# Optimization experiments

Hardware: AMD Instinct MI355X
Metric: run time of the kernel (lower is better)

Reference implementation:

```python
import jax, jax.numpy as jnp
import numpy as np

B, C, H, W = 8, 64, 256, 256
M1, M2 = 16, 16


def setup_inputs() -> dict:
    key = jax.random.key(0)
    k1, k2, k3 = jax.random.split(key, 3)
    scale = 1.0 / (C * C)
    x = jax.random.normal(k1, (B, C, H, W), dtype=jnp.float32)
    # torch.rand(..., dtype=cfloat) -> uniform [0,1) real and imag parts
    w_real = scale * jax.random.uniform(k2, (C, C, M1, M2), dtype=jnp.float32)
    w_imag = scale * jax.random.uniform(k3, (C, C, M1, M2), dtype=jnp.float32)
    return {"x": x, "w_real": w_real, "w_imag": w_imag}


def reference(x, w_real, w_imag):
    m1, m2 = w_real.shape[2], w_real.shape[3]
    h, w = x.shape[-2], x.shape[-1]
    weights = w_real + 1j * w_imag  # (Cin, Cout, m1, m2) complex64
    # rfftn over axes (-1,-2): real->complex transform on the LAST listed axis (-2),
    # so x_ft has shape (B, C, H//2+1, W) — matching torch exactly.
    x_ft = jnp.fft.rfftn(x, axes=(-1, -2))
    out_low = jnp.einsum('bixy,ioxy->boxy', x_ft[..., :m1, :m2], weights)
    out_ft = jnp.zeros_like(x_ft).at[..., :m1, :m2].set(out_low)
    # irfftn with s=(H,W) over default axes (-2,-1): irfft on the last axis
    # truncates it to W//2+1 — same quirky-but-valid behavior as the torch code.
    return jnp.fft.irfftn(out_ft, s=(h, w))
```

## Files before the change

kernel.cpp:

```cpp
#include <hip/hip_runtime.h>
#include <math.h>

#define NIMG 512
#define HW   65536

__global__ __launch_bounds__(256)
void twinit(float* __restrict__ tw_g) {
    int idx = blockIdx.x * 256 + threadIdx.x;
    int n = idx >> 4, k = idx & 15;
    float s, c;
    sincospif(((k * n) & 255) * (1.0f / 128.0f), &s, &c);
    tw_g[idx * 2]     = c;
    tw_g[idx * 2 + 1] = s;
}

__global__ __launch_bounds__(256, 4)
void stageA(const float* __restrict__ x, const float* __restrict__ tw_g,
            float* __restrict__ xf_re, float* __restrict__ xf_im) {
    __shared__ __attribute__((aligned(16))) float tw[2048];
    __shared__ __attribute__((aligned(16))) float cbuf[8192];
    const int tid = threadIdx.x;
    const int img = blockIdx.x;

    ((float4*)tw)[tid]       = ((const float4*)tw_g)[tid];
    ((float4*)tw)[tid + 256] = ((const float4*)tw_g)[tid + 256];
    __syncthreads();

    const float* xp = x + (size_t)img * HW + tid;
    float cr[16], ci[16];
    #pragma unroll
    for (int u = 0; u < 16; ++u) { cr[u] = 0.0f; ci[u] = 0.0f; }

    const float4* tw4 = (const float4*)tw;
    #pragma unroll 2
    for (int hb = 0; hb < 64; ++hb) {
        float a = xp[hb * 256];
        float b = xp[(hb + 64) * 256];
        float c = xp[(hb + 128) * 256];
        float d = xp[(hb + 192) * 256];
        float p = a + c, m = a - c, q = b + d, r = b - d;
        float s0 = p + q, s2 = p - q;
        #pragma unroll
        for (int qq = 0; qq < 8; ++qq) {
            float4 e = tw4[hb * 8 + qq];
            float se = (qq & 1) ? s2 : s0;
            float si = (qq & 1) ? r : -r;
            cr[2*qq]     += se * e.x;
            ci[2*qq]     -= se * e.y;
            cr[2*qq + 1] += m  * e.z + si * e.w;
            ci[2*qq + 1] += si * e.z - m  * e.w;
        }
    }

    float2* cb = (float2*)cbuf;
    #pragma unroll
    for (int u = 0; u < 16; ++u)
        cb[u * 256 + tid] = make_float2(cr[u], ci[u]);
    __syncthreads();

    const int u = tid >> 4, v = tid & 15;
    const bool odd = (v & 1) != 0;
    const float t = (v & 2) ? -1.0f : 1.0f;
    const float2* twc = (const float2*)tw;
    float xr = 0.0f, xi = 0.0f;
    #pragma unroll 2
    for (int wb = 0; wb < 64; ++wb) {
        float2 Ca = cb[u * 256 + wb];
        float2 Cb = cb[u * 256 + wb + 64];
        float2 Cc = cb[u * 256 + wb + 128];
        float2 Cd = cb[u * 256 + wb + 192];
        float pr = Ca.x + Cc.x, pi_ = Ca.y + Cc.y;
        float mr = Ca.x - Cc.x, mi  = Ca.y - Cc.y;
        float qr = Cb.x + Cd.x, qi  = Cb.y + Cd.y;
        float rr = Cb.x - Cd.x, ri  = Cb.y - Cd.y;
        float X1 = odd ? mr : pr;
        float X2 = odd ? ri : qr;
        float Y1 = odd ? mi : pi_;
        float Y2 = odd ? -rr : qi;
        float sr = X1 + t * X2;
        float si = Y1 + t * Y2;
        float2 e = twc[wb * 16 + v];
        xr += sr * e.x + si * e.y;
        xi += si * e.x - sr * e.y;
    }
    xf_re[img * 256 + tid] = xr;
    xf_im[img * 256 + tid] = xi;
}

__global__ __launch_bounds__(256)
void stageB(const float* __restrict__ wr, const float* __restrict__ wi,
            const float* __restrict__ xf_re, const float* __restrict__ xf_im,
            float* __restrict__ s_re, float* __restrict__ s_im) {
    const int tid = threadIdx.x;
    const int o = blockIdx.x >> 3;
    const int b = blockIdx.x & 7;
    float sr = 0.0f, si = 0.0f;
    #pragma unroll 4
    for (int i = 0; i < 64; ++i) {
        float wre = wr[((i * 64 + o) << 8) + tid];
        float wim = wi[((i * 64 + o) << 8) + tid];
        float xr  = xf_re[((b * 64 + i) << 8) + tid];
        float xi  = xf_im[((b * 64 + i) << 8) + tid];
        sr += xr * wre - xi * wim;
        si += xr * wim + xi * wre;
    }
    s_re[((b * 64 + o) << 8) + tid] = sr;
    s_im[((b * 64 + o) << 8) + tid] = si;
}

__global__ __launch_bounds__(256, 4)
void stageC(const float* __restrict__ s_re, const float* __restrict__ s_im,
            const float* __restrict__ tw_g, float* __restrict__ out) {
    __shared__ __attribute__((aligned(16))) float tw[2048];
    __shared__ __attribute__((aligned(16))) float sl[512];
    const int tid = threadIdx.x;
    const int img = blockIdx.x;

    ((float4*)tw)[tid]       = ((const float4*)tw_g)[tid];
    ((float4*)tw)[tid + 256] = ((const float4*)tw_g)[tid + 256];
    {
        int v = tid & 15;
        float scale = (v == 0 ? 1.0f : 2.0f) * (1.0f / 65536.0f);
        sl[tid * 2]     = s_re[img * 256 + tid] * scale;
        sl[tid * 2 + 1] = s_im[img * 256 + tid] * scale;
    }
    __syncthreads();

    float tr[16], ti[16];
    #pragma unroll
    for (int u = 0; u < 16; ++u) { tr[u] = 0.0f; ti[u] = 0.0f; }

    float bs, bc;
    sincospif(tid * (1.0f / 128.0f), &bs, &bc);
    float ec = 1.0f, es = 0.0f;
    for (int v = 0; v < 16; ++v) {
        #pragma unroll
        for (int u = 0; u < 16; ++u) {
            float a = sl[(u * 16 + v) * 2];
            float b = sl[(u * 16 + v) * 2 + 1];
            tr[u] += a * ec - b * es;
            ti[u] += a * es + b * ec;
        }
        float nc = ec * bc - es * bs;
        float ns = ec * bs + es * bc;
        ec = nc; es = ns;
    }

    float* op = out + (size_t)img * HW + tid;
    const float4* tw4 = (const float4*)tw;
    #pragma unroll 2
    for (int hb = 0; hb < 64; ++hb) {
        float o0 = 0.f, o1 = 0.f, o2 = 0.f, o3 = 0.f;
        #pragma unroll
        for (int qq = 0; qq < 8; ++qq) {
            float4 e = tw4[hb * 8 + qq];
            float pre = tr[2*qq]   * e.x - ti[2*qq]   * e.y;
            float pro = tr[2*qq+1] * e.z - ti[2*qq+1] * e.w;
            float pio = tr[2*qq+1] * e.w + ti[2*qq+1] * e.z;
            o0 += pre + pro;
            o2 += pre - pro;
            float g1 = pre - pio, g3 = pre + pio;
            if (qq & 1) { o1 -= g1; o3 -= g3; }
            else        { o1 += g1; o3 += g3; }
        }
        op[hb * 256]         = o0;
        op[(hb + 64) * 256]  = o1;
        op[(hb + 128) * 256] = o2;
        op[(hb + 192) * 256] = o3;
    }
}

extern "C" void kernel_launch(void* const* d_in, const int* in_sizes, int n_in,
                              void* d_out, int out_size, void* d_ws, size_t ws_size,
                              hipStream_t stream) {
    const float* x  = (const float*)d_in[0];
    const float* wr = (const float*)d_in[1];
    const float* wi = (const float*)d_in[2];
    float* out = (float*)d_out;
    float* ws  = (float*)d_ws;

    float* xf_re = ws;
    float* xf_im = ws + 131072;
    float* s_re  = ws + 262144;
    float* s_im  = ws + 393216;
    float* tw_g  = ws + 524288;

    twinit<<<4, 256, 0, stream>>>(tw_g);
    stageA<<<NIMG, 256, 0, stream>>>(x, tw_g, xf_re, xf_im);
    stageB<<<NIMG, 256, 0, stream>>>(wr, wi, xf_re, xf_im, s_re, s_im);
    stageC<<<NIMG, 256, 0, stream>>>(s_re, s_im, tw_g, out);
}
```

Measured before the change: 283.1 us.

## Split row-DFT work across two thread halves and drop twiddle init kernel

Stage A now runs 512 threads per image. Each half accumulates half of the H rows, and the partial sums are reduced through shared memory; the W-direction DFT is then split the same way and reduced once more. Stage C launches two blocks per image, each writing half of the output rows. Both stages compute the twiddle table in-kernel, which removes the separate init launch. This raises parallelism and memory-level concurrency. In exchange it adds more LDS use, extra syncs, and duplicated mode-expansion work in stage C.

New measurement: 355.6 us. +25.6%, slower.

```diff
diff --git a/kernel.cpp b/kernel.cpp
--- a/kernel.cpp
+++ b/kernel.cpp
@@ -4,36 +4,36 @@
 #define NIMG 512
 #define HW   65536
 
-__global__ __launch_bounds__(256)
-void twinit(float* __restrict__ tw_g) {
-    int idx = blockIdx.x * 256 + threadIdx.x;
-    int n = idx >> 4, k = idx & 15;
-    float s, c;
-    sincospif(((k * n) & 255) * (1.0f / 128.0f), &s, &c);
-    tw_g[idx * 2]     = c;
-    tw_g[idx * 2 + 1] = s;
-}
-
-__global__ __launch_bounds__(256, 4)
-void stageA(const float* __restrict__ x, const float* __restrict__ tw_g,
+__global__ __launch_bounds__(512, 4)
+void stageA(const float* __restrict__ x,
             float* __restrict__ xf_re, float* __restrict__ xf_im) {
     __shared__ __attribute__((aligned(16))) float tw[2048];
-    __shared__ __attribute__((aligned(16))) float cbuf[8192];
+    __shared__ __attribute__((aligned(16))) float cb[8192];
+    __shared__ __attribute__((aligned(16))) float cb2[8192];
+    __shared__ __attribute__((aligned(16))) float rbuf[1024];
     const int tid = threadIdx.x;
+    const int t = tid & 255, s = tid >> 8;
     const int img = blockIdx.x;
 
-    ((float4*)tw)[tid]       = ((const float4*)tw_g)[tid];
-    ((float4*)tw)[tid + 256] = ((const float4*)tw_g)[tid + 256];
-    __syncthreads();
-
-    const float* xp = x + (size_t)img * HW + tid;
+    #pragma unroll
+    for (int i = tid; i < 1024; i += 512) {
+        int n = i >> 4, k = i & 15;
+        float sn, cs;
+        sincospif(((k * n) & 255) * (1.0f / 128.0f), &sn, &cs);
+        tw[2 * i] = cs; tw[2 * i + 1] = sn;
+    }
+    __syncthreads();
+
+    const float* xp = x + (size_t)img * HW + t;
     float cr[16], ci[16];
     #pragma unroll
     for (int u = 0; u < 16; ++u) { cr[u] = 0.0f; ci[u] = 0.0f; }
 
     const float4* tw4 = (const float4*)tw;
-    #pragma unroll 2
-    for (int hb = 0; hb < 64; ++hb) {
+    const int hb0 = s << 5;
+    #pragma unroll 4
+    for (int j = 0; j < 32; ++j) {
+        const int hb = hb0 + j;
         float a = xp[hb * 256];
         float b = xp[(hb + 64) * 256];
         float c = xp[(hb + 128) * 256];
@@ -52,23 +52,36 @@
         }
     }
 
-    float2* cb = (float2*)cbuf;
-    #pragma unroll
-    for (int u = 0; u < 16; ++u)
-        cb[u * 256 + tid] = make_float2(cr[u], ci[u]);
-    __syncthreads();
-
-    const int u = tid >> 4, v = tid & 15;
+    float2* cbv  = (float2*)cb;
+    float2* cbv2 = (float2*)cb2;
+    if (s) {
+        #pragma unroll
+        for (int u = 0; u < 16; ++u)
+            cbv2[u * 256 + t] = make_float2(cr[u], ci[u]);
+    }
+    __syncthreads();
+    if (!s) {
+        #pragma unroll
+        for (int u = 0; u < 16; ++u) {
+            float2 o = cbv2[u * 256 + t];
+            cbv[u * 256 + t] = make_float2(cr[u] + o.x, ci[u] + o.y);
+        }
+    }
+    __syncthreads();
+
+    const int u = t >> 4, v = t & 15;
     const bool odd = (v & 1) != 0;
-    const float t = (v & 2) ? -1.0f : 1.0f;
+    const float tsg = (v & 2) ? -1.0f : 1.0f;
     const float2* twc = (const float2*)tw;
     float xr = 0.0f, xi = 0.0f;
+    const int wb0 = s << 5;
     #pragma unroll 2
-    for (int wb = 0; wb < 64; ++wb) {
-        float2 Ca = cb[u * 256 + wb];
-        float2 Cb = cb[u * 256 + wb + 64];
-        float2 Cc = cb[u * 256 + wb + 128];
-        float2 Cd = cb[u * 256 + wb + 192];
+    for (int j = 0; j < 32; ++j) {
+        const int wb = wb0 + j;
+        float2 Ca = cbv[u * 256 + wb];
+        float2 Cb = cbv[u * 256 + wb + 64];
+        float2 Cc = cbv[u * 256 + wb + 128];
+        float2 Cd = cbv[u * 256 + wb + 192];
         float pr = Ca.x + Cc.x, pi_ = Ca.y + Cc.y;
         float mr = Ca.x - Cc.x, mi  = Ca.y - Cc.y;
         float qr = Cb.x + Cd.x, qi  = Cb.y + Cd.y;
@@ -77,14 +90,20 @@
         float X2 = odd ? ri : qr;
         float Y1 = odd ? mi : pi_;
         float Y2 = odd ? -rr : qi;
-        float sr = X1 + t * X2;
-        float si = Y1 + t * Y2;
+        float sr = X1 + tsg * X2;
+        float si = Y1 + tsg * Y2;
         float2 e = twc[wb * 16 + v];
         xr += sr * e.x + si * e.y;
         xi += si * e.x - sr * e.y;
     }
-    xf_re[img * 256 + tid] = xr;
-    xf_im[img * 256 + tid] = xi;
+    float2* rb = (float2*)rbuf;
+    rb[tid] = make_float2(xr, xi);
+    __syncthreads();
+    if (!s) {
+        float2 o = rb[t + 256];
+        xf_re[img * 256 + t] = xr + o.x;
+        xf_im[img * 256 + t] = xi + o.y;
+    }
 }
 
 __global__ __launch_bounds__(256)
@@ -95,7 +114,7 @@
     const int o = blockIdx.x >> 3;
     const int b = blockIdx.x & 7;
     float sr = 0.0f, si = 0.0f;
-    #pragma unroll 4
+    #pragma unroll 8
     for (int i = 0; i < 64; ++i) {
         float wre = wr[((i * 64 + o) << 8) + tid];
         float wim = wi[((i * 64 + o) << 8) + tid];
@@ -110,14 +129,20 @@
 
 __global__ __launch_bounds__(256, 4)
 void stageC(const float* __restrict__ s_re, const float* __restrict__ s_im,
-            const float* __restrict__ tw_g, float* __restrict__ out) {
+            float* __restrict__ out) {
     __shared__ __attribute__((aligned(16))) float tw[2048];
     __shared__ __attribute__((aligned(16))) float sl[512];
     const int tid = threadIdx.x;
-    const int img = blockIdx.x;
-
-    ((float4*)tw)[tid]       = ((const float4*)tw_g)[tid];
-    ((float4*)tw)[tid + 256] = ((const float4*)tw_g)[tid + 256];
+    const int img = blockIdx.x >> 1;
+    const int s   = blockIdx.x & 1;
+
+    #pragma unroll
+    for (int i = tid; i < 1024; i += 256) {
+        int n = i >> 4, k = i & 15;
+        float sn, cs;
+        sincospif(((k * n) & 255) * (1.0f / 128.0f), &sn, &cs);
+        tw[2 * i] = cs; tw[2 * i + 1] = sn;
+    }
     {
         int v = tid & 15;
         float scale = (v == 0 ? 1.0f : 2.0f) * (1.0f / 65536.0f);
@@ -148,8 +173,10 @@
 
     float* op = out + (size_t)img * HW + tid;
     const float4* tw4 = (const float4*)tw;
+    const int hb0 = s << 5;
     #pragma unroll 2
-    for (int hb = 0; hb < 64; ++hb) {
+    for (int j = 0; j < 32; ++j) {
+        const int hb = hb0 + j;
         float o0 = 0.f, o1 = 0.f, o2 = 0.f, o3 = 0.f;
         #pragma unroll
         for (int qq = 0; qq < 8; ++qq) {
@@ -183,10 +210,8 @@
     float* xf_im = ws + 131072;
     float* s_re  = ws + 262144;
     float* s_im  = ws + 393216;
-    float* tw_g  = ws + 524288;
-
-    twinit<<<4, 256, 0, stream>>>(tw_g);
-    stageA<<<NIMG, 256, 0, stream>>>(x, tw_g, xf_re, xf_im);
+
+    stageA<<<NIMG, 512, 0, stream>>>(x, xf_re, xf_im);
     stageB<<<NIMG, 256, 0, stream>>>(wr, wi, xf_re, xf_im, s_re, s_im);
-    stageC<<<NIMG, 256, 0, stream>>>(s_re, s_im, tw_g, out);
-}
+    stageC<<<NIMG * 2, 256, 0, stream>>>(s_re, s_im, out);
+}
```
